# Kernel optimization log

Measured on AMD Instinct MI355X. Metric: run time of the kernel, lower is better.

The kernel has to match this reference:

```python
import jax, jax.numpy as jnp
import numpy as np

DIM = 1024
NUM_HEADS = 16
HEAD_DIM = DIM // NUM_HEADS
B, T = 2, 2048


def _rope_tables(seq_len, head_dim, dtype=jnp.float32):
    inv_freq = 1.0 / (10000.0 ** (jnp.arange(0, head_dim, 2, dtype=jnp.float32) / head_dim))
    t = jnp.arange(seq_len, dtype=jnp.float32)
    freqs = jnp.einsum('i,j->ij', t, inv_freq)            # [T, head_dim/2]
    emb = jnp.concatenate((freqs, freqs), axis=-1)         # [T, head_dim]
    return jnp.cos(emb).astype(dtype), jnp.sin(emb).astype(dtype)


def _rotate_half(x):
    x1, x2 = x[..., : x.shape[-1] // 2], x[..., x.shape[-1] // 2 :]
    return jnp.concatenate((-x2, x1), axis=-1)


def setup_inputs() -> dict:
    key = jax.random.key(0)
    ks = jax.random.split(key, 5)
    s = 1.0 / np.sqrt(DIM)
    return {
        'x': jax.random.normal(ks[0], (B, T, DIM), dtype=jnp.float32),
        'w_q': jax.random.normal(ks[1], (DIM, DIM), dtype=jnp.float32) * s,
        'w_k': jax.random.normal(ks[2], (DIM, DIM), dtype=jnp.float32) * s,
        'w_v': jax.random.normal(ks[3], (DIM, DIM), dtype=jnp.float32) * s,
        'w_out': jax.random.normal(ks[4], (DIM, DIM), dtype=jnp.float32) * s,
    }


def reference(x, w_q, w_k, w_v, w_out):
    Bn, Tn, C = x.shape
    scale = HEAD_DIM ** -0.5
    # nn.Linear(bias=False): y = x @ W^T; reshape to [B, H, T, Dh]
    def proj(w):
        y = jnp.einsum('btc,dc->btd', x, w)
        return y.reshape(Bn, Tn, NUM_HEADS, HEAD_DIM).transpose(0, 2, 1, 3)
    q, k, v = proj(w_q), proj(w_k), proj(w_v)
    cos, sin = _rope_tables(Tn, HEAD_DIM, x.dtype)         # [T, Dh], broadcasts over B,H
    q = q * cos + _rotate_half(q) * sin
    k = k * cos + _rotate_half(k) * sin
    attn = jnp.einsum('bhqd,bhkd->bhqk', q, k) * scale     # [B,H,T,T]
    attn = jax.nn.softmax(attn, axis=-1)
    out = jnp.einsum('bhqk,bhkd->bhqd', attn, v)           # [B,H,T,Dh]
    out = out.transpose(0, 2, 1, 3).reshape(Bn, Tn, C)
    return jnp.einsum('btc,dc->btd', out, w_out)
```

## Files before the change

### kernel.cpp

```cpp
#include <hip/hip_runtime.h>


typedef _Float16 f16;
typedef f16 f16x8 __attribute__((ext_vector_type(8)));
typedef __fp16 fp16x2 __attribute__((ext_vector_type(2)));
typedef float f32x4 __attribute__((ext_vector_type(4)));
typedef float f32x16 __attribute__((ext_vector_type(16)));
typedef unsigned int u32;
typedef unsigned short u16;

union V16 { uint4 u; f16x8 h; };

__device__ __forceinline__ float exp2_fast(float x) {
#if __has_builtin(__builtin_amdgcn_exp2f)
  return __builtin_amdgcn_exp2f(x);
#else
  return __expf(x * 0.69314718056f);
#endif
}

__device__ __forceinline__ u32 pkrtz(float a, float b) {
  union { fp16x2 h; u32 u; } cv;
  cv.h = __builtin_amdgcn_cvt_pkrtz(a, b);
  return cv.u;
}

#define PLSWAP(a, b)                                                          \
  asm volatile("s_nop 1\n\tv_permlane32_swap_b32 %0, %1" : "+v"(a), "+v"(b))

#define GLDS(src, dst) __builtin_amdgcn_global_load_lds(                      \
    (const __attribute__((address_space(1))) void*)(const void*)(src),        \
    (__attribute__((address_space(3))) void*)(void*)(dst), 16, 0, 0)

#define WAITBAR(N) do {                                                       \
    asm volatile("s_waitcnt vmcnt(" #N ")" ::: "memory");                     \
    __builtin_amdgcn_s_barrier();                                             \
    __builtin_amdgcn_sched_barrier(0);                                        \
  } while (0)

__global__ __launch_bounds__(256)
void cvt5_kernel(const float* __restrict__ x,  const float* __restrict__ wq,
                 const float* __restrict__ wk, const float* __restrict__ wv,
                 const float* __restrict__ wo,
                 f16* __restrict__ xh, f16* __restrict__ W3,
                 f16* __restrict__ woh,
                 float* __restrict__ cosT, float* __restrict__ sinT) {
  int bx = blockIdx.x;
  if (bx >= 8192) {
    int i = (bx - 8192) * 256 + threadIdx.x;
    int t = i >> 5, j = i & 31;
    float inv = 1.0f / powf(10000.0f, (float)(2 * j) * (1.0f / 64.0f));
    float ang = (float)t * inv;
    double a = (double)ang;
    cosT[i] = (float)cos(a);
    sinT[i] = (float)sin(a);
    return;
  }
  const float* src; f16* dst; int i;
  if (bx < 4096) {
    src = x; dst = xh; i = bx * 256 + threadIdx.x;
  } else {
    int b = (bx - 4096) >> 10;
    i = ((bx - 4096) & 1023) * 256 + threadIdx.x;
    src = (b == 0) ? wq : (b == 1) ? wk : (b == 2) ? wv : wo;
    dst = (b == 3) ? woh : W3 + (size_t)b * 1048576;
  }
  float4 v = ((const float4*)src)[i];
  union { f16 h[4]; uint2 u; } cv;
  cv.h[0] = (f16)v.x; cv.h[1] = (f16)v.y; cv.h[2] = (f16)v.z; cv.h[3] = (f16)v.w;
  ((uint2*)dst)[i] = cv.u;
}

__global__ __launch_bounds__(256)
void gemm_qkv_kernel(const f16* __restrict__ X,
                     const f16* __restrict__ W3,
                     f16* __restrict__ Qo, f16* __restrict__ Ko,
                     f16* __restrict__ VTo,
                     const float* __restrict__ cosT,
                     const float* __restrict__ sinT) {
  __shared__ u16 lds[3][8192];

  const int tid = threadIdx.x, lane = tid & 63, w = tid >> 6;
  const int wr = w >> 1, wc = w & 1;
  const int c = lane & 15, g = lane >> 4;
  const int bid = blockIdx.x;
  const int r8 = bid & 7, j8 = bid >> 3;
  const int bxd = ((r8 & 3) << 3) + (j8 & 7);
  const int by  = ((r8 >> 2) * 12) + (j8 >> 3);
  const int m0 = bxd * 128;
  const int wsel = by >> 3, hp = by & 7, h0 = hp * 2;
  const f16* Wb = W3 + (size_t)wsel * (1024 * 1024) + (size_t)hp * 128 * 1024;

  const int n1 = tid, n2 = tid + 256;
  const int r1 = n1 >> 2, gc1 = (n1 & 3) ^ ((n1 >> 3) & 3);
  const int r2 = n2 >> 2, gc2 = (n2 & 3) ^ ((n2 >> 3) & 3);
  const f16* gA1 = X + (size_t)(m0 + r1) * 1024 + gc1 * 8;
  const f16* gA2 = X + (size_t)(m0 + r2) * 1024 + gc2 * 8;
  const f16* gB1 = Wb + (size_t)r1 * 1024 + gc1 * 8;
  const f16* gB2 = Wb + (size_t)r2 * 1024 + gc2 * 8;
  const int dA1 = n1 * 8, dA2 = n2 * 8;
  const int dB1 = 4096 + n1 * 8, dB2 = 4096 + n2 * 8;

  f32x4 acc[4][4];
  const f32x4 zero = {0.f, 0.f, 0.f, 0.f};
#pragma unroll
  for (int mi = 0; mi < 4; ++mi)
#pragma unroll
    for (int ni = 0; ni < 4; ++ni) acc[mi][ni] = zero;

#define STAGE_QKV(buf, kt) do {                                               \
    const int ko = (kt) * 32;                                                 \
    GLDS(gA1 + ko, &lds[buf][dA1]);                                           \
    GLDS(gA2 + ko, &lds[buf][dA2]);                                           \
    GLDS(gB1 + ko, &lds[buf][dB1]);                                           \
    GLDS(gB2 + ko, &lds[buf][dB2]);                                           \
  } while (0)

  const int swz = (g ^ ((c >> 1) & 3)) * 8;

  STAGE_QKV(0, 0);
  STAGE_QKV(1, 1);
  WAITBAR(4);

  int cur = 0, nx2 = 2;
  for (int kt = 0; kt < 32; ++kt) {
    if (kt < 30) STAGE_QKV(nx2, kt + 2);
    V16 a[4], b[4];
#pragma unroll
    for (int mi = 0; mi < 4; ++mi)
      a[mi].u = *(const uint4*)&lds[cur][(wr * 64 + mi * 16 + c) * 32 + swz];
#pragma unroll
    for (int ni = 0; ni < 4; ++ni)
      b[ni].u = *(const uint4*)&lds[cur][4096 + (wc * 64 + ni * 16 + c) * 32 + swz];
    __builtin_amdgcn_s_setprio(1);
#pragma unroll
    for (int mi = 0; mi < 4; ++mi)
#pragma unroll
      for (int ni = 0; ni < 4; ++ni)
        acc[mi][ni] = __builtin_amdgcn_mfma_f32_16x16x32_f16(a[mi].h, b[ni].h, acc[mi][ni], 0, 0, 0);
    __builtin_amdgcn_s_setprio(0);
    if (kt < 30) WAITBAR(4); else WAITBAR(0);
    cur = (cur == 2) ? 0 : cur + 1;
    nx2 = (nx2 == 2) ? 0 : nx2 + 1;
  }

  if (wsel < 2) {
    f16* Out = (wsel == 0) ? Qo : Ko;
    const float psc = (wsel == 0) ? 0.18033688f : 1.0f;
    const int head = h0 + wc;
#pragma unroll
    for (int mi = 0; mi < 4; ++mi)
#pragma unroll
      for (int r = 0; r < 4; ++r) {
        int m = m0 + wr * 64 + mi * 16 + g * 4 + r;
        int bb = m >> 11, t = m & 2047;
        float co0 = cosT[t * 32 + c],      si0 = sinT[t * 32 + c];
        float co1 = cosT[t * 32 + 16 + c], si1 = sinT[t * 32 + 16 + c];
#pragma unroll
        for (int ni = 0; ni < 4; ++ni) {
          int d = ni * 16 + c;
          float co = (ni & 1) ? co1 : co0;
          float si = (ni & 1) ? si1 : si0;
          float partner = acc[mi][ni ^ 2][r];
          float v = (acc[mi][ni][r] * co + ((d < 32) ? -partner : partner) * si) * psc;
          Out[((size_t)(bb * 16 + head) * 2048 + t) * 64 + d] = (f16)v;
        }
      }
  } else {
    u16* sT = &lds[0][0];
    const int head = h0 + wc;
    const int bbv = m0 >> 11;
    const int t0 = (m0 & 2047) + wr * 64;
#pragma unroll
    for (int mi = 0; mi < 4; ++mi)
#pragma unroll
      for (int ni = 0; ni < 4; ++ni)
#pragma unroll
        for (int r = 0; r < 4; ++r) {
          int dl = ni * 16 + c;
          int tl = mi * 16 + g * 4 + r;
          union { f16 h; u16 u; } cv; cv.h = (f16)acc[mi][ni][r];
          sT[w * 4608 + dl * 72 + tl] = cv.u;
        }
    f16* dst = VTo + ((size_t)(bbv * 16 + head) * 64 + lane) * 2048 + t0;
    const u16* srcp = &sT[w * 4608 + lane * 72];
#pragma unroll
    for (int s = 0; s < 16; ++s)
      *(uint2*)(dst + s * 4) = *(const uint2*)(srcp + s * 4);
  }
}

__global__ __launch_bounds__(256)
void gemm_out_kernel(const f16* __restrict__ AH, const f16* __restrict__ BH,
                     float* __restrict__ outF) {
  __shared__ u16 lds[3][8192];

  const int tid = threadIdx.x, lane = tid & 63, w = tid >> 6;
  const int wr = w >> 1, wc = w & 1;
  const int c = lane & 15, g = lane >> 4;
  const int bid = blockIdx.x;
  const int r8 = bid & 7, j8 = bid >> 3;
  const int bxd = ((r8 & 3) << 3) + (j8 & 7);
  const int byd = ((r8 >> 2) * 4) + (j8 >> 3);
  const int m0 = bxd * 128, n0 = byd * 128;

  const int n1 = tid, n2 = tid + 256;
  const int r1 = n1 >> 2, gc1 = (n1 & 3) ^ ((n1 >> 3) & 3);
  const int r2 = n2 >> 2, gc2 = (n2 & 3) ^ ((n2 >> 3) & 3);
  const f16* gA1 = AH + (size_t)(m0 + r1) * 1024 + gc1 * 8;
  const f16* gA2 = AH + (size_t)(m0 + r2) * 1024 + gc2 * 8;
  const f16* gB1 = BH + (size_t)(n0 + r1) * 1024 + gc1 * 8;
  const f16* gB2 = BH + (size_t)(n0 + r2) * 1024 + gc2 * 8;
  const int dA1 = n1 * 8, dA2 = n2 * 8;
  const int dB1 = 4096 + n1 * 8, dB2 = 4096 + n2 * 8;

  f32x4 acc[4][4];
  const f32x4 zero = {0.f, 0.f, 0.f, 0.f};
#pragma unroll
  for (int mi = 0; mi < 4; ++mi)
#pragma unroll
    for (int ni = 0; ni < 4; ++ni) acc[mi][ni] = zero;

#define STAGE_OUT(buf, kt) do {                                               \
    const int ko = (kt) * 32;                                                 \
    GLDS(gA1 + ko, &lds[buf][dA1]);                                           \
    GLDS(gA2 + ko, &lds[buf][dA2]);                                           \
    GLDS(gB1 + ko, &lds[buf][dB1]);                                           \
    GLDS(gB2 + ko, &lds[buf][dB2]);                                           \
  } while (0)

  const int swz = (g ^ ((c >> 1) & 3)) * 8;

  STAGE_OUT(0, 0);
  STAGE_OUT(1, 1);
  WAITBAR(4);

  int cur = 0, nx2 = 2;
  for (int kt = 0; kt < 32; ++kt) {
    if (kt < 30) STAGE_OUT(nx2, kt + 2);
    V16 a[4], b[4];
#pragma unroll
    for (int mi = 0; mi < 4; ++mi)
      a[mi].u = *(const uint4*)&lds[cur][(wr * 64 + mi * 16 + c) * 32 + swz];
#pragma unroll
    for (int ni = 0; ni < 4; ++ni)
      b[ni].u = *(const uint4*)&lds[cur][4096 + (wc * 64 + ni * 16 + c) * 32 + swz];
    __builtin_amdgcn_s_setprio(1);
#pragma unroll
    for (int mi = 0; mi < 4; ++mi)
#pragma unroll
      for (int ni = 0; ni < 4; ++ni)
        acc[mi][ni] = __builtin_amdgcn_mfma_f32_16x16x32_f16(a[mi].h, b[ni].h, acc[mi][ni], 0, 0, 0);
    __builtin_amdgcn_s_setprio(0);
    if (kt < 30) WAITBAR(4); else WAITBAR(0);
    cur = (cur == 2) ? 0 : cur + 1;
    nx2 = (nx2 == 2) ? 0 : nx2 + 1;
  }

#pragma unroll
  for (int mi = 0; mi < 4; ++mi)
#pragma unroll
    for (int r = 0; r < 4; ++r) {
      int m = m0 + wr * 64 + mi * 16 + g * 4 + r;
#pragma unroll
      for (int ni = 0; ni < 4; ++ni)
        outF[(size_t)m * 1024 + n0 + wc * 64 + ni * 16 + c] = acc[mi][ni][r];
    }
}

__global__ __launch_bounds__(256, 2)
void attn_kernel(const f16* __restrict__ Q, const f16* __restrict__ K,
                 const f16* __restrict__ VT, f16* __restrict__ OH) {
  __shared__ u16 sKV[3][8192];
  __shared__ u16 sT16[4][32][36];

  const int tid = threadIdx.x, lane = tid & 63, wid = tid >> 6;
  const int q32 = lane & 31, hi = lane >> 5;
  const int bx = blockIdx.x;
  const int bh = (bx & 7) + 8 * (bx >> 7);
  const int qt = (bx >> 3) & 15;
  const int bb = bh >> 4, hh = bh & 15;
  const int q0 = qt * 128 + wid * 32;

  V16 qf[4];
  const f16* qp = Q + ((size_t)bh * 2048 + q0 + q32) * 64 + 8 * hi;
#pragma unroll
  for (int kd = 0; kd < 4; ++kd)
    qf[kd].u = *(const uint4*)(qp + 16 * kd);

  f32x16 o0 = 0.0f, o1 = 0.0f;
  float lsum = 0.f;

  const int srow = tid >> 3, scol = tid & 7;
  const f16* gK = K  + ((size_t)bh * 2048 + srow) * 64 + scol * 8;
  const f16* gV = VT + ((size_t)bh * 64 + srow) * 2048 + scol * 8;
  const int dst0 = srow * 128 + ((scol ^ (srow & 7)) << 4);
  const int dst1 = dst0 + 32 * 128;

  uint4 rk0, rk1, rv0, rv1;
#define LOADT(kt) do {                                                        \
    const f16* pk = gK + (size_t)(kt) * 4096;                                 \
    rk0 = *(const uint4*)(pk);                                                \
    rk1 = *(const uint4*)(pk + 32 * 64);                                      \
    const f16* pv = gV + (size_t)(kt) * 64;                                   \
    rv0 = *(const uint4*)(pv);                                                \
    rv1 = *(const uint4*)(pv + 32 * 2048);                                    \
  } while (0)
#define WRITET(buf) do {                                                      \
    char* base_ = (char*)&sKV[buf][0];                                        \
    *(uint4*)(base_ + dst0) = rk0; *(uint4*)(base_ + dst1) = rk1;             \
    *(uint4*)(base_ + 8192 + dst0) = rv0; *(uint4*)(base_ + 8192 + dst1) = rv1;\
  } while (0)

  const int swzrow = (q32 & 7) << 4;

#define QKT(D0, D1, buf) do {                                                 \
    D0 = 0.0f; D1 = 0.0f;                                                     \
    const char* kb_ = (const char*)&sKV[buf][0];                              \
    __builtin_amdgcn_s_setprio(1);                                            \
    _Pragma("unroll")                                                         \
    for (int kd = 0; kd < 4; ++kd) {                                          \
      const int off = ((32 * kd + 16 * hi) ^ swzrow);                         \
      V16 kf0, kf1;                                                           \
      kf0.u = *(const uint4*)(kb_ + q32 * 128 + off);                         \
      kf1.u = *(const uint4*)(kb_ + (32 + q32) * 128 + off);                  \
      D0 = __builtin_amdgcn_mfma_f32_32x32x16_f16(kf0.h, qf[kd].h, D0, 0, 0, 0);\
      D1 = __builtin_amdgcn_mfma_f32_32x32x16_f16(kf1.h, qf[kd].h, D1, 0, 0, 0);\
    }                                                                         \
    __builtin_amdgcn_s_setprio(0);                                            \
  } while (0)

#define SOFTMAX_PB() do {                                                     \
    u32 c0[8], c1[8];                                                         \
    _Pragma("unroll")                                                         \
    for (int m = 0; m < 8; ++m) {                                             \
      float p0 = exp2_fast(st0[2 * m]);                                       \
      float p1 = exp2_fast(st0[2 * m + 1]);                                   \
      lsum += p0 + p1; c0[m] = pkrtz(p0, p1);                                 \
      float p2 = exp2_fast(st1[2 * m]);                                       \
      float p3 = exp2_fast(st1[2 * m + 1]);                                   \
      lsum += p2 + p3; c1[m] = pkrtz(p2, p3);                                 \
    }                                                                         \
    { u32 y0 = c0[0], x0 = c0[2]; PLSWAP(y0, x0);                             \
      u32 y1 = c0[1], x1 = c0[3]; PLSWAP(y1, x1);                             \
      pB[0].u.x = y0; pB[0].u.y = y1; pB[0].u.z = x0; pB[0].u.w = x1;         \
      u32 y2 = c0[4], x2 = c0[6]; PLSWAP(y2, x2);                             \
      u32 y3 = c0[5], x3 = c0[7]; PLSWAP(y3, x3);                             \
      pB[1].u.x = y2; pB[1].u.y = y3; pB[1].u.z = x2; pB[1].u.w = x3;         \
      u32 y4 = c1[0], x4 = c1[2]; PLSWAP(y4, x4);                             \
      u32 y5 = c1[1], x5 = c1[3]; PLSWAP(y5, x5);                             \
      pB[2].u.x = y4; pB[2].u.y = y5; pB[2].u.z = x4; pB[2].u.w = x5;         \
      u32 y6 = c1[4], x6 = c1[6]; PLSWAP(y6, x6);                             \
      u32 y7 = c1[5], x7 = c1[7]; PLSWAP(y7, x7);                             \
      pB[3].u.x = y6; pB[3].u.y = y7; pB[3].u.z = x6; pB[3].u.w = x7; }       \
  } while (0)

#define PVOP(buf) do {                                                        \
    const char* vb_ = (const char*)&sKV[buf][0] + 8192;                       \
    __builtin_amdgcn_s_setprio(1);                                            \
    _Pragma("unroll")                                                         \
    for (int ks = 0; ks < 4; ++ks) {                                          \
      const int off = ((32 * ks + 16 * hi) ^ swzrow);                         \
      V16 vf0, vf1;                                                           \
      vf0.u = *(const uint4*)(vb_ + q32 * 128 + off);                         \
      vf1.u = *(const uint4*)(vb_ + (32 + q32) * 128 + off);                  \
      o0 = __builtin_amdgcn_mfma_f32_32x32x16_f16(vf0.h, pB[ks].h, o0, 0, 0, 0);\
      o1 = __builtin_amdgcn_mfma_f32_32x32x16_f16(vf1.h, pB[ks].h, o1, 0, 0, 0);\
    }                                                                         \
    __builtin_amdgcn_s_setprio(0);                                            \
  } while (0)

  LOADT(0);
  WRITET(0);
  __syncthreads();
  LOADT(1);
  f32x16 st0, st1;
  QKT(st0, st1, 0);

  V16 pB[4];
  int bw = 1, bp = 0;
  for (int kt = 0; kt < 31; ++kt) {
    WRITET(bw);
    __syncthreads();
    if (kt < 30) LOADT(kt + 2);
    SOFTMAX_PB();
    QKT(st0, st1, bw);
    PVOP(bp);
    bp = bw; bw = (bw == 2) ? 0 : bw + 1;
  }
  SOFTMAX_PB();
  PVOP(bp);

  const float l_run = lsum + __shfl_xor(lsum, 32, 64);
  const float inv = 1.0f / l_run;
  const int qr = lane >> 1, dh = (lane & 1) * 16;
#pragma unroll
  for (int dt = 0; dt < 2; ++dt) {
#pragma unroll
    for (int r = 0; r < 16; ++r) {
      float v = (dt ? o1[r] : o0[r]) * inv;
      union { f16 h; u16 u; } cv; cv.h = (f16)v;
      sT16[wid][q32][(r & 3) + 8 * (r >> 2) + 4 * hi] = cv.u;
    }
    __syncthreads();
    const u16* sp = &sT16[wid][qr][dh];
    uint2 a0 = *(const uint2*)(sp + 0),  a1 = *(const uint2*)(sp + 4);
    uint2 a2 = *(const uint2*)(sp + 8),  a3 = *(const uint2*)(sp + 12);
    size_t gbase = ((size_t)bb * 2048 + q0 + qr) * 1024 + hh * 64 + 32 * dt + dh;
    *(uint2*)(OH + gbase + 0)  = a0;
    *(uint2*)(OH + gbase + 4)  = a1;
    *(uint2*)(OH + gbase + 8)  = a2;
    *(uint2*)(OH + gbase + 12) = a3;
    __syncthreads();
  }
}

extern "C" void kernel_launch(void* const* d_in, const int* in_sizes, int n_in,
                              void* d_out, int out_size, void* d_ws, size_t ws_size,
                              hipStream_t stream) {
  const float* x  = (const float*)d_in[0];
  const float* wq = (const float*)d_in[1];
  const float* wk = (const float*)d_in[2];
  const float* wv = (const float*)d_in[3];
  const float* wo = (const float*)d_in[4];

  constexpr size_t SZ_X   = 4096ull * 1024 * 2;
  constexpr size_t SZ_W   = 1024ull * 1024 * 2;
  constexpr size_t SZ_QKV = 2ull * 16 * 2048 * 64 * 2;
  constexpr size_t SZ_TBL = 2048ull * 32 * 4;
  constexpr size_t NEED = SZ_X + 4 * SZ_W + 3 * SZ_QKV + 2 * SZ_TBL;
  if (ws_size < NEED) return;

  char* ws = (char*)d_ws;
  f16* xh  = (f16*)(ws);
  f16* W3  = (f16*)(ws + SZ_X);
  f16* woh = (f16*)(ws + SZ_X + 3 * SZ_W);
  char* p  = ws + SZ_X + 4 * SZ_W;
  f16* qb  = (f16*)(p);            p += SZ_QKV;
  f16* kb  = (f16*)(p);            p += SZ_QKV;
  f16* vT  = (f16*)(p);            p += SZ_QKV;
  float* cosT = (float*)(p);       p += SZ_TBL;
  float* sinT = (float*)(p);
  f16* oh = xh;

  cvt5_kernel<<<8448, 256, 0, stream>>>(x, wq, wk, wv, wo, xh, W3, woh,
                                        cosT, sinT);

  gemm_qkv_kernel<<<768, 256, 0, stream>>>(xh, W3, qb, kb, vT, cosT, sinT);

  attn_kernel<<<512, 256, 0, stream>>>(qb, kb, vT, oh);

  gemm_out_kernel<<<256, 256, 0, stream>>>(oh, woh, (float*)d_out);
}
```

Baseline: 119.2 us.

## Compute softmax row sums via MFMA and hoist V LDS loads before softmax

```diff
diff --git a/kernel.cpp b/kernel.cpp
--- a/kernel.cpp
+++ b/kernel.cpp
@@ -124,7 +124,6 @@
 
   int cur = 0, nx2 = 2;
   for (int kt = 0; kt < 32; ++kt) {
-    if (kt < 30) STAGE_QKV(nx2, kt + 2);
     V16 a[4], b[4];
 #pragma unroll
     for (int mi = 0; mi < 4; ++mi)
@@ -132,6 +131,7 @@
 #pragma unroll
     for (int ni = 0; ni < 4; ++ni)
       b[ni].u = *(const uint4*)&lds[cur][4096 + (wc * 64 + ni * 16 + c) * 32 + swz];
+    if (kt < 30) STAGE_QKV(nx2, kt + 2);
     __builtin_amdgcn_s_setprio(1);
 #pragma unroll
     for (int mi = 0; mi < 4; ++mi)
@@ -237,7 +237,6 @@
 
   int cur = 0, nx2 = 2;
   for (int kt = 0; kt < 32; ++kt) {
-    if (kt < 30) STAGE_OUT(nx2, kt + 2);
     V16 a[4], b[4];
 #pragma unroll
     for (int mi = 0; mi < 4; ++mi)
@@ -245,6 +244,7 @@
 #pragma unroll
     for (int ni = 0; ni < 4; ++ni)
       b[ni].u = *(const uint4*)&lds[cur][4096 + (wc * 64 + ni * 16 + c) * 32 + swz];
+    if (kt < 30) STAGE_OUT(nx2, kt + 2);
     __builtin_amdgcn_s_setprio(1);
 #pragma unroll
     for (int mi = 0; mi < 4; ++mi)
@@ -288,8 +288,11 @@
   for (int kd = 0; kd < 4; ++kd)
     qf[kd].u = *(const uint4*)(qp + 16 * kd);
 
-  f32x16 o0 = 0.0f, o1 = 0.0f;
-  float lsum = 0.f;
+  V16 onesf;
+  onesf.u.x = 0x3C003C00u; onesf.u.y = 0x3C003C00u;
+  onesf.u.z = 0x3C003C00u; onesf.u.w = 0x3C003C00u;
+
+  f32x16 o0 = 0.0f, o1 = 0.0f, lacc = 0.0f;
 
   const int srow = tid >> 3, scol = tid & 7;
   const f16* gK = K  + ((size_t)bh * 2048 + srow) * 64 + scol * 8;
@@ -336,10 +339,10 @@
     for (int m = 0; m < 8; ++m) {                                             \
       float p0 = exp2_fast(st0[2 * m]);                                       \
       float p1 = exp2_fast(st0[2 * m + 1]);                                   \
-      lsum += p0 + p1; c0[m] = pkrtz(p0, p1);                                 \
+      c0[m] = pkrtz(p0, p1);                                                  \
       float p2 = exp2_fast(st1[2 * m]);                                       \
       float p3 = exp2_fast(st1[2 * m + 1]);                                   \
-      lsum += p2 + p3; c1[m] = pkrtz(p2, p3);                                 \
+      c1[m] = pkrtz(p2, p3);                                                  \
     }                                                                         \
     { u32 y0 = c0[0], x0 = c0[2]; PLSWAP(y0, x0);                             \
       u32 y1 = c0[1], x1 = c0[3]; PLSWAP(y1, x1);                             \
@@ -355,17 +358,23 @@
       pB[3].u.x = y6; pB[3].u.y = y7; pB[3].u.z = x6; pB[3].u.w = x7; }       \
   } while (0)
 
-#define PVOP(buf) do {                                                        \
+#define PVLOAD(buf) do {                                                      \
     const char* vb_ = (const char*)&sKV[buf][0] + 8192;                       \
+    _Pragma("unroll")                                                         \
+    for (int ks = 0; ks < 4; ++ks) {                                          \
+      const int off = ((32 * ks + 16 * hi) ^ swzrow);                         \
+      vf[2 * ks].u     = *(const uint4*)(vb_ + q32 * 128 + off);              \
+      vf[2 * ks + 1].u = *(const uint4*)(vb_ + (32 + q32) * 128 + off);       \
+    }                                                                         \
+  } while (0)
+
+#define PVMM() do {                                                           \
     __builtin_amdgcn_s_setprio(1);                                            \
     _Pragma("unroll")                                                         \
     for (int ks = 0; ks < 4; ++ks) {                                          \
-      const int off = ((32 * ks + 16 * hi) ^ swzrow);                         \
-      V16 vf0, vf1;                                                           \
-      vf0.u = *(const uint4*)(vb_ + q32 * 128 + off);                         \
-      vf1.u = *(const uint4*)(vb_ + (32 + q32) * 128 + off);                  \
-      o0 = __builtin_amdgcn_mfma_f32_32x32x16_f16(vf0.h, pB[ks].h, o0, 0, 0, 0);\
-      o1 = __builtin_amdgcn_mfma_f32_32x32x16_f16(vf1.h, pB[ks].h, o1, 0, 0, 0);\
+      o0 = __builtin_amdgcn_mfma_f32_32x32x16_f16(vf[2 * ks].h, pB[ks].h, o0, 0, 0, 0);\
+      o1 = __builtin_amdgcn_mfma_f32_32x32x16_f16(vf[2 * ks + 1].h, pB[ks].h, o1, 0, 0, 0);\
+      lacc = __builtin_amdgcn_mfma_f32_32x32x16_f16(onesf.h, pB[ks].h, lacc, 0, 0, 0);\
     }                                                                         \
     __builtin_amdgcn_s_setprio(0);                                            \
   } while (0)
@@ -377,22 +386,23 @@
   f32x16 st0, st1;
   QKT(st0, st1, 0);
 
-  V16 pB[4];
+  V16 pB[4], vf[8];
   int bw = 1, bp = 0;
   for (int kt = 0; kt < 31; ++kt) {
     WRITET(bw);
     __syncthreads();
     if (kt < 30) LOADT(kt + 2);
+    PVLOAD(bp);
     SOFTMAX_PB();
     QKT(st0, st1, bw);
-    PVOP(bp);
+    PVMM();
     bp = bw; bw = (bw == 2) ? 0 : bw + 1;
   }
+  PVLOAD(bp);
   SOFTMAX_PB();
-  PVOP(bp);
-
-  const float l_run = lsum + __shfl_xor(lsum, 32, 64);
-  const float inv = 1.0f / l_run;
+  PVMM();
+
+  const float inv = 1.0f / lacc[0];
   const int qr = lane >> 1, dh = (lane & 1) * 16;
 #pragma unroll
   for (int dt = 0; dt < 2; ++dt) {
```

Result: no change. 120.2 us (+0.8%).
